# Performance work log

Measured on AMD Instinct MI355X. Metric: run time of the kernel, lower is better.

The kernel has to match this reference:

```python
import jax, jax.numpy as jnp
import numpy as np

NEG_INF = -1e9


def setup_inputs() -> dict:
    key = jax.random.key(0)
    k1, k2, k3 = jax.random.split(key, 3)
    B, N, F_IN, F_OUT = 8, 4096, 128, 64
    h = jax.random.normal(k1, (B, N, F_IN), dtype=jnp.float32)
    # xavier_uniform with gain=1.414 on [F_IN, F_OUT]
    limit = 1.414 * np.sqrt(6.0 / (F_IN + F_OUT))
    W = jax.random.uniform(k2, (F_IN, F_OUT), dtype=jnp.float32, minval=-limit, maxval=limit)
    adj = jax.random.randint(k3, (N, N), 0, 2, dtype=jnp.int32)
    return {"h": h, "W": W, "adj": adj}


def reference(h, W, adj):
    # h: [B, N, F_in], W: [F_in, F_out], adj: [N, N]
    F_out = W.shape[1]
    Wh = jnp.einsum('bnf,fo->bno', h, W)                      # [B, N, F_out]
    scores = jnp.einsum('bnd,bmd->bnm', Wh, Wh) / np.sqrt(F_out).astype(np.float32)
    attention = jnp.where(adj[None, :, :] > 0, scores, NEG_INF)
    attention = jax.nn.softmax(attention, axis=2)             # [B, N, N]
    # dropout p=0.0 / eval mode -> identity
    h_prime = jnp.einsum('bnm,bmd->bnd', attention, Wh)       # [B, N, F_out]
    return jax.nn.elu(h_prime)  # concat=True path
```

## Files before the change

kernel.cpp:

```cpp
#include <hip/hip_runtime.h>

typedef _Float16 half8  __attribute__((ext_vector_type(8)));
typedef _Float16 half4v __attribute__((ext_vector_type(4)));
typedef float    float4v __attribute__((ext_vector_type(4)));

#define N_ 4096
#define B_ 8
#define D_ 64
#define F_ 128

__global__ __launch_bounds__(256) void pack_adj_kernel(const int* __restrict__ adj,
                                                       unsigned long long* __restrict__ bits) {
  int i = blockIdx.x * 256 + threadIdx.x;
  unsigned long long m = __ballot(adj[i] > 0);
  if ((threadIdx.x & 63) == 0) bits[i >> 6] = m;
}

__global__ __launch_bounds__(256) void wh_kernel(const float* __restrict__ h,
                                                 const float* __restrict__ W,
                                                 _Float16* __restrict__ Wh16) {
  __shared__ __align__(16) float    hs[64][132];
  __shared__ __align__(16) _Float16 wt[64][132];
  const int t = threadIdx.x;
  const int rowbase = blockIdx.x * 64;
  const float4v* hg = (const float4v*)(h + (size_t)rowbase * F_);
#pragma unroll
  for (int k = 0; k < 8; ++k) {
    int i4 = t + k * 256;
    float4v v = hg[i4];
    int r = i4 >> 5, c4 = (i4 & 31) * 4;
    *(float4v*)&hs[r][c4] = v;
  }
#pragma unroll
  for (int k = 0; k < 8; ++k) {
    int i4 = t + k * 256;
    float4v v = ((const float4v*)W)[i4];
    int f = i4 >> 4, c4 = (i4 & 15) * 4;
    wt[c4 + 0][f] = (_Float16)v[0];
    wt[c4 + 1][f] = (_Float16)v[1];
    wt[c4 + 2][f] = (_Float16)v[2];
    wt[c4 + 3][f] = (_Float16)v[3];
  }
  __syncthreads();
  const int w = t >> 6, lane = t & 63;
  const int r0 = w * 16;
  float acc[16];
#pragma unroll
  for (int i = 0; i < 16; ++i) acc[i] = 0.f;
#pragma unroll 4
  for (int f4 = 0; f4 < 32; ++f4) {
    half4v wv = *(half4v*)&wt[lane][f4 * 4];
    float w0 = (float)wv[0], w1 = (float)wv[1], w2 = (float)wv[2], w3 = (float)wv[3];
#pragma unroll
    for (int i = 0; i < 16; ++i) {
      float4v hv = *(float4v*)&hs[r0 + i][f4 * 4];
      acc[i] += hv[0] * w0 + hv[1] * w1 + hv[2] * w2 + hv[3] * w3;
    }
  }
#pragma unroll
  for (int i = 0; i < 16; ++i)
    Wh16[(size_t)(rowbase + r0 + i) * D_ + lane] = (_Float16)acc[i];
}

__global__ __launch_bounds__(256) void tr_kernel(const _Float16* __restrict__ Wh16,
                                                 _Float16* __restrict__ WhT16) {
  __shared__ __align__(16) _Float16 tl[64][72];
  int bid = blockIdx.x;
  int b  = bid >> 6;
  int kb = (bid & 63) * 64;
  int t  = threadIdx.x;
  int kl = t >> 2, c0 = (t & 3) * 16;
  const _Float16* src = Wh16 + ((size_t)(b * N_ + kb + kl)) * D_ + c0;
  *(half8*)&tl[kl][c0]     = *(const half8*)src;
  *(half8*)&tl[kl][c0 + 8] = *(const half8*)(src + 8);
  __syncthreads();
  int dl = t >> 2, k0 = (t & 3) * 16;
  half8 o0, o1;
#pragma unroll
  for (int i = 0; i < 8; ++i) o0[i] = tl[k0 + i][dl];
#pragma unroll
  for (int i = 0; i < 8; ++i) o1[i] = tl[k0 + 8 + i][dl];
  _Float16* dst = WhT16 + ((size_t)(b * D_ + dl)) * N_ + kb + k0;
  *(half8*)dst       = o0;
  *(half8*)(dst + 8) = o1;
}

__global__ __launch_bounds__(512, 4) void attn_kernel(
    const unsigned long long* __restrict__ bits,
    const _Float16* __restrict__ Wh,
    const _Float16* __restrict__ WhT,
    float* __restrict__ out) {
  __shared__ __align__(16) char lds[49152];
  const int tid  = threadIdx.x;
  const int w    = tid >> 6;
  const int lane = tid & 63;
  const int g    = lane >> 4;
  const int c    = lane & 15;
  const int qi   = w & 3;
  const int s    = w >> 2;
  const int bid  = blockIdx.x;
  const int b    = bid >> 6;
  const int q0b  = (bid & 63) * 64;
  const int q0w  = q0b + qi * 16;

  const _Float16* Whb  = Wh  + (size_t)b * N_ * D_;
  const _Float16* WhTb = WhT + (size_t)b * D_ * N_;
  _Float16* Kst = (_Float16*)(lds + s * 8192);
  _Float16* Vst = (_Float16*)(lds + 16384 + s * 8192);
  char* Pb = lds + 32768 + w * 2048;

  const int e0  = (qi * 2 + 0) * 64 + lane;
  const int e1  = (qi * 2 + 1) * 64 + lane;
  const int r0e = e0 >> 3, s0e = (e0 & 7) ^ (r0e & 7);
  const int r1e = e1 >> 3, s1e = (e1 & 7) ^ (r1e & 7);

  half8 qf[2];
#pragma unroll
  for (int ds = 0; ds < 2; ++ds) {
    half8 v = *(const half8*)(Whb + (size_t)(q0w + c) * D_ + ds * 32 + g * 8);
    qf[ds] = v * (_Float16)0.125f;
  }

  float4v o_acc[4];
#pragma unroll
  for (int d = 0; d < 4; ++d) o_acc[d] = (float4v){0.f, 0.f, 0.f, 0.f};
  float mrow = -1e30f, lrow = 0.f;

  const unsigned long long* bq = bits + (size_t)(q0w + c) * 64 + s * 32;

  int k0n = (s * 32) * 64;
  half8 ka = *(const half8*)(Whb + (size_t)(k0n + r0e) * D_ + s0e * 8);
  half8 kb = *(const half8*)(Whb + (size_t)(k0n + r1e) * D_ + s1e * 8);
  half8 va = *(const half8*)(WhTb + (size_t)r0e * N_ + k0n + s0e * 8);
  half8 vb = *(const half8*)(WhTb + (size_t)r1e * N_ + k0n + s1e * 8);
  unsigned long long bw = bq[0];

  for (int t = 0; t < 32; ++t) {
    __syncthreads();
    *(half8*)(Kst + e0 * 8) = ka;
    *(half8*)(Kst + e1 * 8) = kb;
    *(half8*)(Vst + e0 * 8) = va;
    *(half8*)(Vst + e1 * 8) = vb;
    __syncthreads();

    const int t1 = (t + 1 < 32) ? t + 1 : 31;
    k0n = (s * 32 + t1) * 64;
    ka = *(const half8*)(Whb + (size_t)(k0n + r0e) * D_ + s0e * 8);
    kb = *(const half8*)(Whb + (size_t)(k0n + r1e) * D_ + s1e * 8);
    va = *(const half8*)(WhTb + (size_t)r0e * N_ + k0n + s0e * 8);
    vb = *(const half8*)(WhTb + (size_t)r1e * N_ + k0n + s1e * 8);
    unsigned long long bwn = bq[t1];

    float4v sac[4];
#pragma unroll
    for (int st = 0; st < 4; ++st) {
      const _Float16* kr = Kst + (st * 16 + c) * 64;
      half8 kf0 = *(const half8*)(kr + ((g       ^ (c & 7)) * 8));
      half8 kf1 = *(const half8*)(kr + (((g + 4) ^ (c & 7)) * 8));
      float4v z = (float4v){0.f, 0.f, 0.f, 0.f};
      z = __builtin_amdgcn_mfma_f32_16x16x32_f16(kf0, qf[0], z, 0, 0, 0);
      z = __builtin_amdgcn_mfma_f32_16x16x32_f16(kf1, qf[1], z, 0, 0, 0);
      sac[st] = z;
    }

    float tmax = -1e30f;
#pragma unroll
    for (int st = 0; st < 4; ++st) {
      unsigned wb = (unsigned)(bw >> (st * 16 + g * 4));
#pragma unroll
      for (int j = 0; j < 4; ++j) {
        float v = (wb & (1u << j)) ? sac[st][j] : -1e9f;
        sac[st][j] = v;
        tmax = fmaxf(tmax, v);
      }
    }
    tmax = fmaxf(tmax, __shfl_xor(tmax, 16));
    tmax = fmaxf(tmax, __shfl_xor(tmax, 32));

    float mnew  = fmaxf(mrow, tmax);
    float alpha = __expf(mrow - mnew);
    mrow = mnew;
    lrow *= alpha;
#pragma unroll
    for (int j = 0; j < 4; ++j) {
      float aj = __shfl(alpha, (lane & 48) | (g * 4 + j));
#pragma unroll
      for (int d = 0; d < 4; ++d) o_acc[d][j] *= aj;
    }

#pragma unroll
    for (int st = 0; st < 4; ++st) {
      float p0 = __expf(sac[st][0] - mrow);
      float p1 = __expf(sac[st][1] - mrow);
      float p2 = __expf(sac[st][2] - mrow);
      float p3 = __expf(sac[st][3] - mrow);
      lrow += (p0 + p1) + (p2 + p3);
      uint2 pr;
      pr.x = __builtin_bit_cast(unsigned, __builtin_amdgcn_cvt_pkrtz(p0, p1));
      pr.y = __builtin_bit_cast(unsigned, __builtin_amdgcn_cvt_pkrtz(p2, p3));
      const int cell = st * 2 + (g >> 1);
      *(uint2*)(Pb + (cell * 16 + c) * 16 + (g & 1) * 8) = pr;
    }

#pragma unroll
    for (int ks = 0; ks < 2; ++ks) {
      half8 af = *(const half8*)(Pb + ((ks * 4 + g) * 16 + c) * 16);
#pragma unroll
      for (int d = 0; d < 4; ++d) {
        const int vrow = d * 16 + c;
        half8 vf = *(const half8*)(Vst + vrow * 64 + (((ks * 4 + g) ^ (c & 7)) * 8));
        o_acc[d] = __builtin_amdgcn_mfma_f32_16x16x32_f16(af, vf, o_acc[d], 0, 0, 0);
      }
    }
    bw = bwn;
  }

  lrow += __shfl_xor(lrow, 16);
  lrow += __shfl_xor(lrow, 32);
  __syncthreads();
  float* Ob = (float*)lds;
#pragma unroll
  for (int d = 0; d < 4; ++d)
#pragma unroll
    for (int j = 0; j < 4; ++j)
      Ob[(w * 16 + g * 4 + j) * 66 + d * 16 + c] = o_acc[d][j];
  float2* mlb = (float2*)(lds + 36864);
  if (g == 0) mlb[w * 16 + c] = make_float2(mrow, lrow);
  __syncthreads();

#pragma unroll
  for (int it = 0; it < 8; ++it) {
    int r   = w + it * 8;
    int col = lane;
    int qq = r >> 4, rl = r & 15;
    float2 ml0 = mlb[qq * 16 + rl];
    float2 ml1 = mlb[(qq + 4) * 16 + rl];
    float mm = fmaxf(ml0.x, ml1.x);
    float a0 = __expf(ml0.x - mm);
    float a1 = __expf(ml1.x - mm);
    float l  = a0 * ml0.y + a1 * ml1.y;
    float o  = a0 * Ob[(qq * 16 + rl) * 66 + col] + a1 * Ob[((qq + 4) * 16 + rl) * 66 + col];
    float x  = o / l;
    x = x > 0.f ? x : (__expf(x) - 1.f);
    out[((size_t)b * N_ + q0b + r) * D_ + col] = x;
  }
}

extern "C" void kernel_launch(void* const* d_in, const int* in_sizes, int n_in,
                              void* d_out, int out_size, void* d_ws, size_t ws_size,
                              hipStream_t stream) {
  const float* h = (const float*)d_in[0];
  const float* W = (const float*)d_in[1];
  const int* adj = (const int*)d_in[2];
  float* out = (float*)d_out;

  char* ws = (char*)d_ws;
  unsigned long long* bits = (unsigned long long*)ws;
  _Float16* Wh16  = (_Float16*)(ws + (2u << 20));
  _Float16* WhT16 = (_Float16*)(ws + (6u << 20));

  hipLaunchKernelGGL(pack_adj_kernel, dim3((N_ * N_) / 256), dim3(256), 0, stream, adj, bits);
  hipLaunchKernelGGL(wh_kernel,   dim3((B_ * N_) / 64), dim3(256), 0, stream, h, W, Wh16);
  hipLaunchKernelGGL(tr_kernel,   dim3(B_ * (N_ / 64)), dim3(256), 0, stream, Wh16, WhT16);
  hipLaunchKernelGGL(attn_kernel, dim3(B_ * (N_ / 64)), dim3(512), 0, stream, bits, Wh16, WhT16, out);
}
```

Before: 212.3 us.

## Fuse transpose into Wh kernel, split attention keys four ways, read V from global

The Wh kernel now also writes the transposed WhT tile through an LDS tile, so the separate transpose launch goes away. The attention kernel changes to 32 queries per block with four key splits of 16 tiles each, which doubles the grid. It stages only K in LDS and loads V fragments directly from global memory. Softmax switches to exp2 with log2(e) folded into the query scale, and the occupancy hint rises to 6. The per-block V reuse from LDS is lost, and the uncached global V reads may add memory latency.

Result: slower. 332.2 us (+56.4%).

```diff
diff --git a/kernel.cpp b/kernel.cpp
--- a/kernel.cpp
+++ b/kernel.cpp
@@ -18,9 +18,11 @@
 
 __global__ __launch_bounds__(256) void wh_kernel(const float* __restrict__ h,
                                                  const float* __restrict__ W,
-                                                 _Float16* __restrict__ Wh16) {
+                                                 _Float16* __restrict__ Wh16,
+                                                 _Float16* __restrict__ WhT16) {
   __shared__ __align__(16) float    hs[64][132];
   __shared__ __align__(16) _Float16 wt[64][132];
+  __shared__ __align__(16) _Float16 otile[64][72];
   const int t = threadIdx.x;
   const int rowbase = blockIdx.x * 64;
   const float4v* hg = (const float4v*)(h + (size_t)rowbase * F_);
@@ -58,34 +60,25 @@
     }
   }
 #pragma unroll
-  for (int i = 0; i < 16; ++i)
-    Wh16[(size_t)(rowbase + r0 + i) * D_ + lane] = (_Float16)acc[i];
-}
-
-__global__ __launch_bounds__(256) void tr_kernel(const _Float16* __restrict__ Wh16,
-                                                 _Float16* __restrict__ WhT16) {
-  __shared__ __align__(16) _Float16 tl[64][72];
-  int bid = blockIdx.x;
-  int b  = bid >> 6;
-  int kb = (bid & 63) * 64;
-  int t  = threadIdx.x;
-  int kl = t >> 2, c0 = (t & 3) * 16;
-  const _Float16* src = Wh16 + ((size_t)(b * N_ + kb + kl)) * D_ + c0;
-  *(half8*)&tl[kl][c0]     = *(const half8*)src;
-  *(half8*)&tl[kl][c0 + 8] = *(const half8*)(src + 8);
-  __syncthreads();
-  int dl = t >> 2, k0 = (t & 3) * 16;
+  for (int i = 0; i < 16; ++i) {
+    _Float16 hv = (_Float16)acc[i];
+    Wh16[(size_t)(rowbase + r0 + i) * D_ + lane] = hv;
+    otile[r0 + i][lane] = hv;
+  }
+  __syncthreads();
+  const int dl = t >> 2, k0t = (t & 3) * 16;
   half8 o0, o1;
 #pragma unroll
-  for (int i = 0; i < 8; ++i) o0[i] = tl[k0 + i][dl];
-#pragma unroll
-  for (int i = 0; i < 8; ++i) o1[i] = tl[k0 + 8 + i][dl];
-  _Float16* dst = WhT16 + ((size_t)(b * D_ + dl)) * N_ + kb + k0;
+  for (int i = 0; i < 8; ++i) o0[i] = otile[k0t + i][dl];
+#pragma unroll
+  for (int i = 0; i < 8; ++i) o1[i] = otile[k0t + 8 + i][dl];
+  const int b = rowbase >> 12, n0 = rowbase & 4095;
+  _Float16* dst = WhT16 + ((size_t)(b * D_ + dl)) * N_ + n0 + k0t;
   *(half8*)dst       = o0;
   *(half8*)(dst + 8) = o1;
 }
 
-__global__ __launch_bounds__(512, 4) void attn_kernel(
+__global__ __launch_bounds__(512, 6) void attn_kernel(
     const unsigned long long* __restrict__ bits,
     const _Float16* __restrict__ Wh,
     const _Float16* __restrict__ WhT,
@@ -96,29 +89,32 @@
   const int lane = tid & 63;
   const int g    = lane >> 4;
   const int c    = lane & 15;
-  const int qi   = w & 3;
-  const int s    = w >> 2;
+  const int qi   = w & 1;
+  const int s    = w >> 1;
   const int bid  = blockIdx.x;
-  const int b    = bid >> 6;
-  const int q0b  = (bid & 63) * 64;
+  const int b    = bid >> 7;
+  const int q0b  = (bid & 127) * 32;
   const int q0w  = q0b + qi * 16;
 
   const _Float16* Whb  = Wh  + (size_t)b * N_ * D_;
   const _Float16* WhTb = WhT + (size_t)b * D_ * N_;
   _Float16* Kst = (_Float16*)(lds + s * 8192);
-  _Float16* Vst = (_Float16*)(lds + 16384 + s * 8192);
   char* Pb = lds + 32768 + w * 2048;
 
-  const int e0  = (qi * 2 + 0) * 64 + lane;
-  const int e1  = (qi * 2 + 1) * 64 + lane;
-  const int r0e = e0 >> 3, s0e = (e0 & 7) ^ (r0e & 7);
-  const int r1e = e1 >> 3, s1e = (e1 & 7) ^ (r1e & 7);
+  const int li = qi * 64 + lane;
+  int er[4], es[4];
+#pragma unroll
+  for (int i = 0; i < 4; ++i) {
+    int e = li + i * 128;
+    er[i] = e >> 3;
+    es[i] = (e & 7) ^ (er[i] & 7);
+  }
 
   half8 qf[2];
 #pragma unroll
   for (int ds = 0; ds < 2; ++ds) {
     half8 v = *(const half8*)(Whb + (size_t)(q0w + c) * D_ + ds * 32 + g * 8);
-    qf[ds] = v * (_Float16)0.125f;
+    qf[ds] = v * (_Float16)0.18033688f;
   }
 
   float4v o_acc[4];
@@ -126,29 +122,28 @@
   for (int d = 0; d < 4; ++d) o_acc[d] = (float4v){0.f, 0.f, 0.f, 0.f};
   float mrow = -1e30f, lrow = 0.f;
 
-  const unsigned long long* bq = bits + (size_t)(q0w + c) * 64 + s * 32;
-
-  int k0n = (s * 32) * 64;
-  half8 ka = *(const half8*)(Whb + (size_t)(k0n + r0e) * D_ + s0e * 8);
-  half8 kb = *(const half8*)(Whb + (size_t)(k0n + r1e) * D_ + s1e * 8);
-  half8 va = *(const half8*)(WhTb + (size_t)r0e * N_ + k0n + s0e * 8);
-  half8 vb = *(const half8*)(WhTb + (size_t)r1e * N_ + k0n + s1e * 8);
+  const unsigned long long* bq = bits + (size_t)(q0w + c) * 64 + s * 16;
+
+  int k0n = (s * 16) * 64;
+  half8 kpre[4];
+#pragma unroll
+  for (int i = 0; i < 4; ++i)
+    kpre[i] = *(const half8*)(Whb + (size_t)(k0n + er[i]) * D_ + es[i] * 8);
   unsigned long long bw = bq[0];
 
-  for (int t = 0; t < 32; ++t) {
+  for (int t = 0; t < 16; ++t) {
     __syncthreads();
-    *(half8*)(Kst + e0 * 8) = ka;
-    *(half8*)(Kst + e1 * 8) = kb;
-    *(half8*)(Vst + e0 * 8) = va;
-    *(half8*)(Vst + e1 * 8) = vb;
+#pragma unroll
+    for (int i = 0; i < 4; ++i)
+      *(half8*)(Kst + (li + i * 128) * 8) = kpre[i];
     __syncthreads();
 
-    const int t1 = (t + 1 < 32) ? t + 1 : 31;
-    k0n = (s * 32 + t1) * 64;
-    ka = *(const half8*)(Whb + (size_t)(k0n + r0e) * D_ + s0e * 8);
-    kb = *(const half8*)(Whb + (size_t)(k0n + r1e) * D_ + s1e * 8);
-    va = *(const half8*)(WhTb + (size_t)r0e * N_ + k0n + s0e * 8);
-    vb = *(const half8*)(WhTb + (size_t)r1e * N_ + k0n + s1e * 8);
+    const int kc = (s * 16 + t) * 64;
+    const int t1 = (t + 1 < 16) ? t + 1 : 15;
+    k0n = (s * 16 + t1) * 64;
+#pragma unroll
+    for (int i = 0; i < 4; ++i)
+      kpre[i] = *(const half8*)(Whb + (size_t)(k0n + er[i]) * D_ + es[i] * 8);
     unsigned long long bwn = bq[t1];
 
     float4v sac[4];
@@ -178,7 +173,7 @@
     tmax = fmaxf(tmax, __shfl_xor(tmax, 32));
 
     float mnew  = fmaxf(mrow, tmax);
-    float alpha = __expf(mrow - mnew);
+    float alpha = exp2f(mrow - mnew);
     mrow = mnew;
     lrow *= alpha;
 #pragma unroll
@@ -190,10 +185,10 @@
 
 #pragma unroll
     for (int st = 0; st < 4; ++st) {
-      float p0 = __expf(sac[st][0] - mrow);
-      float p1 = __expf(sac[st][1] - mrow);
-      float p2 = __expf(sac[st][2] - mrow);
-      float p3 = __expf(sac[st][3] - mrow);
+      float p0 = exp2f(sac[st][0] - mrow);
+      float p1 = exp2f(sac[st][1] - mrow);
+      float p2 = exp2f(sac[st][2] - mrow);
+      float p3 = exp2f(sac[st][3] - mrow);
       lrow += (p0 + p1) + (p2 + p3);
       uint2 pr;
       pr.x = __builtin_bit_cast(unsigned, __builtin_amdgcn_cvt_pkrtz(p0, p1));
@@ -207,8 +202,7 @@
       half8 af = *(const half8*)(Pb + ((ks * 4 + g) * 16 + c) * 16);
 #pragma unroll
       for (int d = 0; d < 4; ++d) {
-        const int vrow = d * 16 + c;
-        half8 vf = *(const half8*)(Vst + vrow * 64 + (((ks * 4 + g) ^ (c & 7)) * 8));
+        half8 vf = *(const half8*)(WhTb + (size_t)(d * 16 + c) * N_ + kc + ks * 32 + g * 8);
         o_acc[d] = __builtin_amdgcn_mfma_f32_16x16x32_f16(af, vf, o_acc[d], 0, 0, 0);
       }
     }
@@ -223,24 +217,31 @@
   for (int d = 0; d < 4; ++d)
 #pragma unroll
     for (int j = 0; j < 4; ++j)
-      Ob[(w * 16 + g * 4 + j) * 66 + d * 16 + c] = o_acc[d][j];
-  float2* mlb = (float2*)(lds + 36864);
+      Ob[(w * 16 + g * 4 + j) * 64 + d * 16 + c] = o_acc[d][j];
+  float2* mlb = (float2*)(lds + 32768);
   if (g == 0) mlb[w * 16 + c] = make_float2(mrow, lrow);
   __syncthreads();
 
 #pragma unroll
-  for (int it = 0; it < 8; ++it) {
-    int r   = w + it * 8;
-    int col = lane;
+  for (int it = 0; it < 4; ++it) {
+    int idx = tid + it * 512;
+    int r = idx >> 6, col = idx & 63;
     int qq = r >> 4, rl = r & 15;
-    float2 ml0 = mlb[qq * 16 + rl];
-    float2 ml1 = mlb[(qq + 4) * 16 + rl];
-    float mm = fmaxf(ml0.x, ml1.x);
-    float a0 = __expf(ml0.x - mm);
-    float a1 = __expf(ml1.x - mm);
-    float l  = a0 * ml0.y + a1 * ml1.y;
-    float o  = a0 * Ob[(qq * 16 + rl) * 66 + col] + a1 * Ob[((qq + 4) * 16 + rl) * 66 + col];
-    float x  = o / l;
+    float2 ml[4];
+    float mm = -1e30f;
+#pragma unroll
+    for (int p = 0; p < 4; ++p) {
+      ml[p] = mlb[(p * 2 + qq) * 16 + rl];
+      mm = fmaxf(mm, ml[p].x);
+    }
+    float l = 0.f, o = 0.f;
+#pragma unroll
+    for (int p = 0; p < 4; ++p) {
+      float a = exp2f(ml[p].x - mm);
+      l += a * ml[p].y;
+      o += a * Ob[((p * 2 + qq) * 16 + rl) * 64 + col];
+    }
+    float x = o / l;
     x = x > 0.f ? x : (__expf(x) - 1.f);
     out[((size_t)b * N_ + q0b + r) * D_ + col] = x;
   }
@@ -260,7 +261,6 @@
   _Float16* WhT16 = (_Float16*)(ws + (6u << 20));
 
   hipLaunchKernelGGL(pack_adj_kernel, dim3((N_ * N_) / 256), dim3(256), 0, stream, adj, bits);
-  hipLaunchKernelGGL(wh_kernel,   dim3((B_ * N_) / 64), dim3(256), 0, stream, h, W, Wh16);
-  hipLaunchKernelGGL(tr_kernel,   dim3(B_ * (N_ / 64)), dim3(256), 0, stream, Wh16, WhT16);
-  hipLaunchKernelGGL(attn_kernel, dim3(B_ * (N_ / 64)), dim3(512), 0, stream, bits, Wh16, WhT16, out);
-}
+  hipLaunchKernelGGL(wh_kernel,   dim3((B_ * N_) / 64), dim3(256), 0, stream, h, W, Wh16, WhT16);
+  hipLaunchKernelGGL(attn_kernel, dim3(B_ * (N_ / 32)), dim3(512), 0, stream, bits, Wh16, WhT16, out);
+}
```
